# Kernel tuning notes

Measured on AMD Instinct MI355X. Metric: run time of the kernel, lower is better.

## Reference

```python
import jax, jax.numpy as jnp
import numpy as np

EPS = 1e-5

def rmsnorm(x, w, eps=EPS):
    # torch-style RMSNorm: x / rms(x) * weight
    return x * jax.lax.rsqrt(jnp.mean(x * x, axis=-1, keepdims=True) + eps) * w

def setup_inputs() -> dict:
    key = jax.random.key(0)
    k1, k2 = jax.random.split(key)
    B, T, D, Q, K = 8, 1024, 1024, 8, 4096
    d = D // Q
    x = jax.random.normal(k1, (B, T, D), dtype=jnp.float32)
    codebooks = jax.random.normal(k2, (Q, K, d), dtype=jnp.float32)
    input_norm_w = jnp.ones((D,), dtype=jnp.float32)
    output_norm_w = jnp.ones((D,), dtype=jnp.float32)
    return {"x": x, "codebooks": codebooks,
            "input_norm_w": input_norm_w, "output_norm_w": output_norm_w}

def reference(x, codebooks, input_norm_w, output_norm_w):
    B, T, D = x.shape
    Q, K, d = codebooks.shape
    xn = rmsnorm(x, input_norm_w)
    xq = xn.reshape(B, T, Q, d)  # split hidden into Q sub-vectors
    # squared euclidean distances (argmin equal to cdist argmin)
    x2 = jnp.sum(xq * xq, axis=-1, keepdims=True)          # [B,T,Q,1]
    c2 = jnp.sum(codebooks * codebooks, axis=-1)           # [Q,K]
    xc = jnp.einsum('btqd,qkd->btqk', xq, codebooks)       # [B,T,Q,K]
    d2 = x2 - 2.0 * xc + c2[None, None]                    # [B,T,Q,K]
    idx = jnp.argmin(d2, axis=-1)                          # [B,T,Q] int
    # gather nearest code per quantizer: equivalent of stacked embedding lookups
    quant = codebooks[jnp.arange(Q)[None, None, :], idx]   # [B,T,Q,d]
    quant = quant.reshape(B, T, D)
    out = rmsnorm(quant, output_norm_w)
    return out, idx
```

## Files before the change

### kernel.cpp

```cpp
#include <hip/hip_runtime.h>
#include <math.h>
#include <float.h>

#define Q_     8
#define K_     4096
#define dd_    128
#define D_     1024
#define ROWS   8192
#define NCHUNK 64
#define NCH_L  32
#define TAU    0.02f

typedef __attribute__((ext_vector_type(8))) _Float16 f16x8;
typedef __attribute__((ext_vector_type(4))) float f32x4;
typedef __attribute__((ext_vector_type(4))) unsigned int u32x4;

typedef const __attribute__((address_space(1))) unsigned int* gas_p;
typedef __attribute__((address_space(3))) unsigned int* las_p;

__device__ inline unsigned f2u(float x) { union { float f; unsigned u; } v; v.f = x; return v.u; }
__device__ inline float u2f(unsigned x) { union { unsigned u; float f; } v; v.u = x; return v.f; }
__device__ inline unsigned short f2h(float x) {
    union { _Float16 h; unsigned short u; } v; v.h = (_Float16)x; return v.u;
}
__device__ inline unsigned umin_(unsigned a, unsigned b) { return a < b ? a : b; }
__device__ inline unsigned umax_(unsigned a, unsigned b) { return a > b ? a : b; }
__device__ inline unsigned fflip(float x) {
    unsigned u = f2u(x);
    return (u & 0x80000000u) ? ~u : (u | 0x80000000u);
}
__device__ inline unsigned long long shfl_xor_u64(unsigned long long v, int m) {
    unsigned lo = (unsigned)v, hi = (unsigned)(v >> 32);
    lo = __shfl_xor(lo, m, 64);
    hi = __shfl_xor(hi, m, 64);
    return ((unsigned long long)hi << 32) | lo;
}

__global__ void k_prep(const float* __restrict__ cb, const float* __restrict__ x,
                       const float* __restrict__ w, float* __restrict__ xn,
                       unsigned short* __restrict__ panels, float* __restrict__ c2h,
                       float* __restrict__ x2h, int* __restrict__ cntF, int* __restrict__ cntS) {
    const int bid = blockIdx.x, t = threadIdx.x;
    if (bid == 0 && t == 0) { *cntF = 0; *cntS = 0; }
    if (bid < NCHUNK * Q_) {
        int c = bid & 63, q = bid >> 6;
        const float* src = cb + ((size_t)q * K_ + c * 64) * dd_;
        unsigned short* dst = panels + (size_t)(q * NCHUNK + c) * 8192;
        #pragma unroll
        for (int i = 0; i < 4; i++) {
            int sid = i * 256 + t;
            int n = sid >> 4, j = sid & 15;
            const float* sp = src + n * dd_ + j * 8;
            f32x4 v0 = *(const f32x4*)sp;
            f32x4 v1 = *(const f32x4*)(sp + 4);
            float xs[8] = {v0.x, v0.y, v0.z, v0.w, v1.x, v1.y, v1.z, v1.w};
            unsigned short hb[8];
            float ss = 0.0f;
            #pragma unroll
            for (int e = 0; e < 8; e++) {
                float xv = -xs[e];
                ss = fmaf(xv, xv, ss);
                hb[e] = f2h(xv);
            }
            int slot = j ^ (n & 15);
            u32x4 H;
            H.x = (unsigned)hb[0] | ((unsigned)hb[1] << 16);
            H.y = (unsigned)hb[2] | ((unsigned)hb[3] << 16);
            H.z = (unsigned)hb[4] | ((unsigned)hb[5] << 16);
            H.w = (unsigned)hb[6] | ((unsigned)hb[7] << 16);
            *(u32x4*)&dst[(n * 16 + slot) * 8] = H;
            ss += __shfl_xor(ss, 1, 64);
            ss += __shfl_xor(ss, 2, 64);
            ss += __shfl_xor(ss, 4, 64);
            ss += __shfl_xor(ss, 8, 64);
            if (j == 0) c2h[q * K_ + c * 64 + n] = 0.5f * ss;
        }
    } else {
        int row = bid - NCHUNK * Q_;
        const float4 v = *(const float4*)(x + (size_t)row * D_ + t * 4);
        float ss = v.x * v.x + v.y * v.y + v.z * v.z + v.w * v.w;
        #pragma unroll
        for (int o = 32; o > 0; o >>= 1) ss += __shfl_xor(ss, o, 64);
        __shared__ float acc[4];
        if ((t & 63) == 0) acc[t >> 6] = ss;
        __syncthreads();
        float tot = (acc[0] + acc[1]) + (acc[2] + acc[3]);
        float sc  = 1.0f / sqrtf(tot * (1.0f / D_) + 1e-5f);
        const float4 wv = *(const float4*)(w + t * 4);
        float4 o;
        o.x = v.x * sc * wv.x; o.y = v.y * sc * wv.y;
        o.z = v.z * sc * wv.z; o.w = v.w * sc * wv.w;
        *(float4*)(xn + (size_t)row * D_ + t * 4) = o;
        float so = o.x * o.x + o.y * o.y + o.z * o.z + o.w * o.w;
        so += __shfl_xor(so, 1, 64);
        so += __shfl_xor(so, 2, 64);
        so += __shfl_xor(so, 4, 64);
        so += __shfl_xor(so, 8, 64);
        so += __shfl_xor(so, 16, 64);
        if ((t & 31) == 0) x2h[row * Q_ + (t >> 5)] = 0.5f * so;
    }
}

__launch_bounds__(256, 2)
__global__ void k_dist(const float* __restrict__ xn, const unsigned short* __restrict__ panels,
                       const float* __restrict__ c2h, const float* __restrict__ x2h,
                       unsigned* __restrict__ recs) {
    __shared__ char smem[36864];

    const int t    = threadIdx.x;
    const int lane = t & 63, wave = t >> 6;
    const int wm = wave >> 1, wn = wave & 1;
    const int col = lane & 15, quad = lane >> 4;
    const int q = blockIdx.y;
    const int z = blockIdx.z;
    const int row0 = blockIdx.x * 128;

    f16x8 ah[4][4], al[4][4];
    #pragma unroll
    for (int mt = 0; mt < 4; mt++) {
        #pragma unroll
        for (int kt = 0; kt < 4; kt++) {
            const float* ap = xn + (size_t)(row0 + wm * 64 + mt * 16 + col) * D_
                              + q * dd_ + kt * 32 + quad * 8;
            f32x4 v0 = *(const f32x4*)ap;
            f32x4 v1 = *(const f32x4*)(ap + 4);
            #pragma unroll
            for (int e = 0; e < 8; e++) {
                float xv = (e < 4) ? v0[e] : v1[e - 4];
                _Float16 h = (_Float16)xv;
                float r = xv - (float)h;
                ah[mt][kt][e] = h;
                al[mt][kt][e] = (_Float16)r;
            }
        }
    }

    f32x4 x2v[4];
    #pragma unroll
    for (int mt = 0; mt < 4; mt++)
        #pragma unroll
        for (int r = 0; r < 4; r++)
            x2v[mt][r] = x2h[(size_t)(row0 + wm * 64 + mt * 16 + quad * 4 + r) * Q_ + q];

    unsigned m1[16], m2[16];
    #pragma unroll
    for (int i = 0; i < 16; i++) { m1[i] = 0xFFFFFFFFu; m2[i] = 0xFFFFFFFFu; }

    const size_t panq = (size_t)q * NCHUNK * 8192 + (size_t)z * NCH_L * 8192;
    const float* c2hq = c2h + q * K_ + z * (NCH_L * 64);

    {
        const unsigned short* src = panels + panq;
        #pragma unroll
        for (int i = 0; i < 4; i++) {
            int boff = i * 4096 + t * 16;
            __builtin_amdgcn_global_load_lds((gas_p)((const char*)src + boff),
                                             (las_p)(smem + boff), 16, 0, 0);
        }
    }
    float ch0 = c2hq[wn * 32 + col];
    float ch1 = c2hq[wn * 32 + col + 16];

    for (int c = 0; c < NCH_L; c++) {
        __syncthreads();
        if (c + 1 < NCH_L) {
            const unsigned short* src = panels + panq + (size_t)(c + 1) * 8192;
            char* stage = smem + ((c + 1) & 1) * 16384;
            #pragma unroll
            for (int i = 0; i < 4; i++) {
                int boff = i * 4096 + t * 16;
                __builtin_amdgcn_global_load_lds((gas_p)((const char*)src + boff),
                                                 (las_p)(stage + boff), 16, 0, 0);
            }
        }
        float ch0n = 0.0f, ch1n = 0.0f;
        if (c + 1 < NCH_L) {
            ch0n = c2hq[(c + 1) * 64 + wn * 32 + col];
            ch1n = c2hq[(c + 1) * 64 + wn * 32 + col + 16];
        }
        const char* cbuf = smem + (c & 1) * 16384;

        f32x4 acc[4][2];
        #pragma unroll
        for (int mt = 0; mt < 4; mt++) {
            acc[mt][0] = x2v[mt] + ch0;
            acc[mt][1] = x2v[mt] + ch1;
        }

        #pragma unroll
        for (int kt = 0; kt < 4; kt++) {
            const int sw = ((quad + kt * 4) ^ col) * 16;
            const int a0 = (wn * 32 + col) * 256 + sw;
            const int a1 = a0 + 4096;
            f16x8 b0 = *(const f16x8*)(cbuf + a0);
            f16x8 b1 = *(const f16x8*)(cbuf + a1);
            #pragma unroll
            for (int mt = 0; mt < 4; mt++) {
                acc[mt][0] = __builtin_amdgcn_mfma_f32_16x16x32_f16(ah[mt][kt], b0, acc[mt][0], 0, 0, 0);
                acc[mt][0] = __builtin_amdgcn_mfma_f32_16x16x32_f16(al[mt][kt], b0, acc[mt][0], 0, 0, 0);
                acc[mt][1] = __builtin_amdgcn_mfma_f32_16x16x32_f16(ah[mt][kt], b1, acc[mt][1], 0, 0, 0);
                acc[mt][1] = __builtin_amdgcn_mfma_f32_16x16x32_f16(al[mt][kt], b1, acc[mt][1], 0, 0, 0);
            }
        }

        const unsigned tg0 = (unsigned)((z * NCH_L + c) << 1), tg1 = tg0 | 1u;
        #pragma unroll
        for (int mt = 0; mt < 4; mt++) {
            #pragma unroll
            for (int r = 0; r < 4; r++) {
                const int sl = mt * 4 + r;
                unsigned p0 = (f2u(acc[mt][0][r]) & 0xFFFFFF80u) | tg0;
                unsigned p1 = (f2u(acc[mt][1][r]) & 0xFFFFFF80u) | tg1;
                unsigned pmin = umin_(p0, p1), pmax = umax_(p0, p1);
                m2[sl] = umin_(umin_(m2[sl], umax_(m1[sl], pmin)), pmax);
                m1[sl] = umin_(m1[sl], pmin);
            }
        }
        ch0 = ch0n; ch1 = ch1n;
    }

    __syncthreads();
    unsigned* rm1 = (unsigned*)smem;
    unsigned* rm2 = (unsigned*)(smem + 16896);
    #pragma unroll
    for (int mt = 0; mt < 4; mt++) {
        #pragma unroll
        for (int r = 0; r < 4; r++) {
            int sl = mt * 4 + r;
            int row_l = wm * 64 + mt * 16 + quad * 4 + r;
            int e = wn * 16 + col;
            rm1[row_l * 33 + e] = m1[sl];
            rm2[row_l * 33 + e] = m2[sl];
        }
    }
    __syncthreads();
    if (t < 128) {
        unsigned b1 = 0xFFFFFFFFu;
        int be = 0;
        for (int e = 0; e < 32; e++) {
            unsigned v1 = rm1[t * 33 + e];
            if (v1 < b1) { b1 = v1; be = e; }
        }
        float f1  = u2f(b1 & 0xFFFFFF80u);
        float thr = f1 + TAU;
        int ns = 0, fb = 0;
        unsigned sv0 = 0xFFFFFFFFu, sk0 = 0, sv1 = 0xFFFFFFFFu, sk1 = 0;
        for (int e = 0; e < 32; e++) {
            unsigned v2m = rm2[t * 33 + e] & 0xFFFFFF80u;
            if (u2f(v2m) < thr) fb = 1;
            if (e != be) {
                unsigned v1 = rm1[t * 33 + e];
                unsigned vm = v1 & 0xFFFFFF80u;
                if (u2f(vm) < thr) {
                    unsigned tg = v1 & 0x7Fu;
                    unsigned kk = ((tg >> 1) << 6) | (((unsigned)e >> 4) << 5)
                                | ((tg & 1u) << 4) | ((unsigned)e & 15u);
                    if (ns == 0)      { sv0 = vm; sk0 = kk; }
                    else if (ns == 1) { sv1 = vm; sk1 = kk; }
                    ns++;
                }
            }
        }
        if (ns > 2) fb = 1;
        unsigned tg1x = b1 & 0x7Fu;
        unsigned k1 = ((tg1x >> 1) << 6) | (((unsigned)be >> 4) << 5)
                    | ((tg1x & 1u) << 4) | ((unsigned)be & 15u);
        int item = (row0 + t) * Q_ + q;
        unsigned* rec = recs + ((size_t)item * 2 + z) * 8;
        rec[0] = b1 & 0xFFFFFF80u;
        rec[1] = k1;
        rec[2] = (unsigned)ns | ((unsigned)fb << 8);
        rec[3] = 0;
        rec[4] = sv0; rec[5] = sk0;
        rec[6] = sv1; rec[7] = sk1;
    }
}

__global__ void k_merge(const unsigned* __restrict__ recs, int* __restrict__ idxi,
                        float* __restrict__ idxf, int* __restrict__ listF, int* __restrict__ cntF,
                        int* __restrict__ srl, int* __restrict__ cntS,
                        unsigned long long* __restrict__ resc) {
    int item = blockIdx.x * blockDim.x + threadIdx.x;
    if (item >= ROWS * Q_) return;
    const unsigned* ra = recs + (size_t)item * 16;
    const unsigned* rb = ra + 8;
    unsigned m1a = ra[0], m1b = rb[0];
    bool awin = m1a <= m1b;
    unsigned mw = awin ? m1a : m1b;
    unsigned kw = awin ? ra[1] : rb[1];
    unsigned ml = awin ? m1b : m1a;
    unsigned kl = awin ? rb[1] : ra[1];
    float thr = u2f(mw) + TAU;
    int fb = (int)(((ra[2] | rb[2]) >> 8) & 1u);

    bool q0 = u2f(ml) < thr;
    int nsa = (int)(ra[2] & 0xFFu), nsb = (int)(rb[2] & 0xFFu);
    bool qa0 = (nsa > 0) && (u2f(ra[4]) < thr);
    bool qa1 = (nsa > 1) && (u2f(ra[6]) < thr);
    bool qb0 = (nsb > 0) && (u2f(rb[4]) < thr);
    bool qb1 = (nsb > 1) && (u2f(rb[6]) < thr);
    int nr = (int)q0 + (int)qa0 + (int)qa1 + (int)qb0 + (int)qb1;

    idxi[item] = (int)kw;
    idxf[item] = (float)kw;
    if (fb) {
        resc[item] = 0xFFFFFFFFFFFFFFFFull;
        int p = atomicAdd(cntF, 1);
        listF[p] = item;
    } else if (nr > 0) {
        int p = atomicAdd(cntS, 1);
        int* e = srl + (size_t)p * 8;
        e[0] = item; e[1] = nr + 1; e[2] = (int)kw;
        int o = 3;
        if (q0)  e[o++] = (int)kl;
        if (qa0) e[o++] = (int)ra[5];
        if (qa1) e[o++] = (int)ra[7];
        if (qb0) e[o++] = (int)rb[5];
        if (qb1) e[o++] = (int)rb[7];
    }
}

__global__ void k_rescue(const float* __restrict__ xn, const float* __restrict__ cb,
                         const float* __restrict__ c2h, const int* __restrict__ listF,
                         const int* __restrict__ cntF, const int* __restrict__ srl,
                         const int* __restrict__ cntS,
                         unsigned long long* __restrict__ resc,
                         int* __restrict__ idxi, float* __restrict__ idxf) {
    __shared__ float xq[dd_];
    __shared__ unsigned long long kshare[8];
    const int t = threadIdx.x;
    if (blockIdx.x < 2048) {
        const int n = *cntF;
        const int seg = blockIdx.x & 7;
        for (int ii = blockIdx.x >> 3; ii < n; ii += 256) {
            __syncthreads();
            int item = listF[ii];
            int rg = item >> 3, q = item & 7;
            if (t < dd_) xq[t] = xn[(size_t)rg * D_ + q * dd_ + t];
            __syncthreads();
            unsigned long long best = 0xFFFFFFFFFFFFFFFFull;
            #pragma unroll
            for (int i = 0; i < 2; i++) {
                int k = seg * 512 + i * 256 + t;
                const float* cp = cb + ((size_t)q * K_ + k) * dd_;
                float dot = 0.0f;
                #pragma unroll 8
                for (int d = 0; d < dd_; d += 4) {
                    f32x4 cv = *(const f32x4*)(cp + d);
                    dot = fmaf(cv.x, xq[d],     dot);
                    dot = fmaf(cv.y, xq[d + 1], dot);
                    dot = fmaf(cv.z, xq[d + 2], dot);
                    dot = fmaf(cv.w, xq[d + 3], dot);
                }
                float s = c2h[q * K_ + k] - dot;
                unsigned long long key = ((unsigned long long)fflip(s) << 32) | (unsigned)k;
                best = best < key ? best : key;
            }
            #pragma unroll
            for (int o = 32; o > 0; o >>= 1) {
                unsigned long long other = shfl_xor_u64(best, o);
                best = best < other ? best : other;
            }
            if ((t & 63) == 0) kshare[t >> 6] = best;
            __syncthreads();
            if (t == 0) {
                unsigned long long b = kshare[0];
                b = b < kshare[1] ? b : kshare[1];
                b = b < kshare[2] ? b : kshare[2];
                b = b < kshare[3] ? b : kshare[3];
                atomicMin(&resc[item], b);
            }
        }
    } else {
        const int n = *cntS;
        for (int ii = (int)blockIdx.x - 2048; ii < n; ii += 2048) {
            __syncthreads();
            const int* e = srl + (size_t)ii * 8;
            int item = e[0], nc = e[1];
            int rg = item >> 3, q = item & 7;
            if (t < dd_) xq[t] = xn[(size_t)rg * D_ + q * dd_ + t];
            __syncthreads();
            int g = t >> 5, l = t & 31;
            unsigned long long key = 0xFFFFFFFFFFFFFFFFull;
            if (g < nc) {
                int k = e[2 + g];
                const float* cp = cb + ((size_t)q * K_ + k) * dd_ + l * 4;
                f32x4 cv = *(const f32x4*)cp;
                float dot = cv.x * xq[l * 4]     + cv.y * xq[l * 4 + 1]
                          + cv.z * xq[l * 4 + 2] + cv.w * xq[l * 4 + 3];
                dot += __shfl_xor(dot, 16, 64);
                dot += __shfl_xor(dot, 8, 64);
                dot += __shfl_xor(dot, 4, 64);
                dot += __shfl_xor(dot, 2, 64);
                dot += __shfl_xor(dot, 1, 64);
                float s = c2h[q * K_ + k] - dot;
                key = ((unsigned long long)fflip(s) << 32) | (unsigned)k;
            }
            if (l == 0) kshare[g] = key;
            __syncthreads();
            if (t == 0) {
                unsigned long long b = kshare[0];
                #pragma unroll
                for (int gg = 1; gg < 8; gg++) b = b < kshare[gg] ? b : kshare[gg];
                int k = (int)(unsigned)(b & 0xFFFFFFFFull);
                idxi[item] = k;
                idxf[item] = (float)k;
            }
        }
    }
}

__global__ void k_fin(const int* __restrict__ listF, const int* __restrict__ cntF,
                      const unsigned long long* __restrict__ resc,
                      int* __restrict__ idxi, float* __restrict__ idxf) {
    const int n = *cntF;
    for (int i = blockIdx.x * blockDim.x + threadIdx.x; i < n; i += gridDim.x * blockDim.x) {
        int item = listF[i];
        int k = (int)(unsigned)(resc[item] & 0xFFFFFFFFull);
        idxi[item] = k;
        idxf[item] = (float)k;
    }
}

__global__ void k_out(const float* __restrict__ cb, const int* __restrict__ idx_i,
                      const float* __restrict__ w, float* __restrict__ out) {
    int row = blockIdx.x;
    int t   = threadIdx.x;
    __shared__ int   sidx[Q_];
    __shared__ float acc[4];
    if (t < Q_) sidx[t] = idx_i[row * Q_ + t];
    __syncthreads();
    int col = t * 4;
    int q   = col >> 7;
    int dc  = col & 127;
    const float4 v = *(const float4*)(cb + ((size_t)q * K_ + sidx[q]) * dd_ + dc);
    float ss = v.x * v.x + v.y * v.y + v.z * v.z + v.w * v.w;
    #pragma unroll
    for (int o = 32; o > 0; o >>= 1) ss += __shfl_xor(ss, o, 64);
    if ((t & 63) == 0) acc[t >> 6] = ss;
    __syncthreads();
    float tot = (acc[0] + acc[1]) + (acc[2] + acc[3]);
    float sc  = 1.0f / sqrtf(tot * (1.0f / D_) + 1e-5f);
    const float4 wv = *(const float4*)(w + col);
    float4 o;
    o.x = v.x * sc * wv.x; o.y = v.y * sc * wv.y;
    o.z = v.z * sc * wv.z; o.w = v.w * sc * wv.w;
    *(float4*)(out + (size_t)row * D_ + col) = o;
}

extern "C" void kernel_launch(void* const* d_in, const int* in_sizes, int n_in,
                              void* d_out, int out_size, void* d_ws, size_t ws_size,
                              hipStream_t stream) {
    const float* x     = (const float*)d_in[0];
    const float* cb    = (const float*)d_in[1];
    const float* w_in  = (const float*)d_in[2];
    const float* w_out = (const float*)d_in[3];

    float* out  = (float*)d_out;
    float* idxf = out + (size_t)ROWS * D_;

    unsigned short* panels = (unsigned short*)d_ws;
    float* c2h  = (float*)((char*)d_ws + (8u << 20));
    float* x2h  = c2h + Q_ * K_;
    unsigned long long* resc = (unsigned long long*)(x2h + (size_t)ROWS * Q_);
    int*   idxi = (int*)(resc + (size_t)ROWS * Q_);
    int*   listF = idxi + ROWS * Q_;
    unsigned* recs = (unsigned*)(listF + ROWS * Q_);
    int*   srl  = (int*)(recs + (size_t)ROWS * Q_ * 16);
    int*   cntF = srl + (size_t)ROWS * Q_ * 8;
    int*   cntS = cntF + 1;

    k_prep  <<<dim3(NCHUNK * Q_ + ROWS), 256, 0, stream>>>(cb, x, w_in, out, panels, c2h, x2h, cntF, cntS);
    k_dist  <<<dim3(ROWS / 128, Q_, 2),  256, 0, stream>>>(out, panels, c2h, x2h, recs);
    k_merge <<<dim3(ROWS * Q_ / 256),    256, 0, stream>>>(recs, idxi, idxf, listF, cntF, srl, cntS, resc);
    k_rescue<<<dim3(4096),               256, 0, stream>>>(out, cb, c2h, listF, cntF, srl, cntS, resc, idxi, idxf);
    k_fin   <<<dim3(64),                 256, 0, stream>>>(listF, cntF, resc, idxi, idxf);
    k_out   <<<dim3(ROWS),               256, 0, stream>>>(cb, idxi, w_out, out);
}
```

Before: 246.7 us.

## Triple-buffer codebook panels with explicit vmcnt waits and stage c2 in LDS

Changes the k_dist main loop from double-buffered to triple-buffered LDS staging, prefetching two chunks ahead. It replaces __syncthreads with manual s_waitcnt vmcnt and s_barrier so one chunk's loads stay in flight across the barrier. The c2 norms are copied into LDS once and added after the MFMA chain rather than in the accumulator init, and MFMA sections get raised wave priority. Shared memory grows from 36KB to 56KB, which may reduce occupancy below the two-blocks launch bound.

```diff
diff --git a/kernel.cpp b/kernel.cpp
--- a/kernel.cpp
+++ b/kernel.cpp
@@ -105,7 +105,7 @@
 __global__ void k_dist(const float* __restrict__ xn, const unsigned short* __restrict__ panels,
                        const float* __restrict__ c2h, const float* __restrict__ x2h,
                        unsigned* __restrict__ recs) {
-    __shared__ char smem[36864];
+    __shared__ char smem[57344];
 
     const int t    = threadIdx.x;
     const int lane = t & 63, wave = t >> 6;
@@ -147,48 +147,61 @@
     for (int i = 0; i < 16; i++) { m1[i] = 0xFFFFFFFFu; m2[i] = 0xFFFFFFFFu; }
 
     const size_t panq = (size_t)q * NCHUNK * 8192 + (size_t)z * NCH_L * 8192;
-    const float* c2hq = c2h + q * K_ + z * (NCH_L * 64);
+    const float* c2s = (const float*)(smem + 49152);
 
     {
-        const unsigned short* src = panels + panq;
-        #pragma unroll
-        for (int i = 0; i < 4; i++) {
+        const char* c2src = (const char*)(c2h + (size_t)q * K_ + (size_t)z * (NCH_L * 64));
+        #pragma unroll
+        for (int i = 0; i < 2; i++) {
             int boff = i * 4096 + t * 16;
-            __builtin_amdgcn_global_load_lds((gas_p)((const char*)src + boff),
-                                             (las_p)(smem + boff), 16, 0, 0);
-        }
-    }
-    float ch0 = c2hq[wn * 32 + col];
-    float ch1 = c2hq[wn * 32 + col + 16];
-
-    for (int c = 0; c < NCH_L; c++) {
-        __syncthreads();
-        if (c + 1 < NCH_L) {
-            const unsigned short* src = panels + panq + (size_t)(c + 1) * 8192;
-            char* stage = smem + ((c + 1) & 1) * 16384;
+            __builtin_amdgcn_global_load_lds((gas_p)(c2src + boff),
+                                             (las_p)(smem + 49152 + boff), 16, 0, 0);
+        }
+        #pragma unroll
+        for (int b = 0; b < 2; b++) {
+            const char* src = (const char*)(panels + panq + (size_t)b * 8192);
             #pragma unroll
             for (int i = 0; i < 4; i++) {
                 int boff = i * 4096 + t * 16;
-                __builtin_amdgcn_global_load_lds((gas_p)((const char*)src + boff),
+                __builtin_amdgcn_global_load_lds((gas_p)(src + boff),
+                                                 (las_p)(smem + b * 16384 + boff), 16, 0, 0);
+            }
+        }
+    }
+    asm volatile("s_waitcnt vmcnt(4)" ::: "memory");
+    __builtin_amdgcn_s_barrier();
+
+    for (int c = 0; c < NCH_L; c++) {
+        const char* cbuf = smem + (c % 3) * 16384;
+        if (c + 2 < NCH_L) {
+            const char* src = (const char*)(panels + panq + (size_t)(c + 2) * 8192);
+            char* stage = smem + ((c + 2) % 3) * 16384;
+            #pragma unroll
+            for (int i = 0; i < 4; i++) {
+                int boff = i * 4096 + t * 16;
+                __builtin_amdgcn_global_load_lds((gas_p)(src + boff),
                                                  (las_p)(stage + boff), 16, 0, 0);
             }
         }
-        float ch0n = 0.0f, ch1n = 0.0f;
-        if (c + 1 < NCH_L) {
-            ch0n = c2hq[(c + 1) * 64 + wn * 32 + col];
-            ch1n = c2hq[(c + 1) * 64 + wn * 32 + col + 16];
-        }
-        const char* cbuf = smem + (c & 1) * 16384;
 
         f32x4 acc[4][2];
-        #pragma unroll
-        for (int mt = 0; mt < 4; mt++) {
-            acc[mt][0] = x2v[mt] + ch0;
-            acc[mt][1] = x2v[mt] + ch1;
-        }
-
-        #pragma unroll
-        for (int kt = 0; kt < 4; kt++) {
+        __builtin_amdgcn_s_setprio(1);
+        {
+            const int sw = (quad ^ col) * 16;
+            const int a0 = (wn * 32 + col) * 256 + sw;
+            const int a1 = a0 + 4096;
+            f16x8 b0 = *(const f16x8*)(cbuf + a0);
+            f16x8 b1 = *(const f16x8*)(cbuf + a1);
+            #pragma unroll
+            for (int mt = 0; mt < 4; mt++) {
+                acc[mt][0] = __builtin_amdgcn_mfma_f32_16x16x32_f16(ah[mt][0], b0, x2v[mt], 0, 0, 0);
+                acc[mt][0] = __builtin_amdgcn_mfma_f32_16x16x32_f16(al[mt][0], b0, acc[mt][0], 0, 0, 0);
+                acc[mt][1] = __builtin_amdgcn_mfma_f32_16x16x32_f16(ah[mt][0], b1, x2v[mt], 0, 0, 0);
+                acc[mt][1] = __builtin_amdgcn_mfma_f32_16x16x32_f16(al[mt][0], b1, acc[mt][1], 0, 0, 0);
+            }
+        }
+        #pragma unroll
+        for (int kt = 1; kt < 4; kt++) {
             const int sw = ((quad + kt * 4) ^ col) * 16;
             const int a0 = (wn * 32 + col) * 256 + sw;
             const int a1 = a0 + 4096;
@@ -202,21 +215,30 @@
                 acc[mt][1] = __builtin_amdgcn_mfma_f32_16x16x32_f16(al[mt][kt], b1, acc[mt][1], 0, 0, 0);
             }
         }
-
+        __builtin_amdgcn_s_setprio(0);
+
+        const float ch0 = c2s[c * 64 + wn * 32 + col];
+        const float ch1 = c2s[c * 64 + wn * 32 + col + 16];
         const unsigned tg0 = (unsigned)((z * NCH_L + c) << 1), tg1 = tg0 | 1u;
         #pragma unroll
         for (int mt = 0; mt < 4; mt++) {
             #pragma unroll
             for (int r = 0; r < 4; r++) {
                 const int sl = mt * 4 + r;
-                unsigned p0 = (f2u(acc[mt][0][r]) & 0xFFFFFF80u) | tg0;
-                unsigned p1 = (f2u(acc[mt][1][r]) & 0xFFFFFF80u) | tg1;
+                unsigned p0 = (f2u(acc[mt][0][r] + ch0) & 0xFFFFFF80u) | tg0;
+                unsigned p1 = (f2u(acc[mt][1][r] + ch1) & 0xFFFFFF80u) | tg1;
                 unsigned pmin = umin_(p0, p1), pmax = umax_(p0, p1);
                 m2[sl] = umin_(umin_(m2[sl], umax_(m1[sl], pmin)), pmax);
                 m1[sl] = umin_(m1[sl], pmin);
             }
         }
-        ch0 = ch0n; ch1 = ch1n;
+
+        if (c + 2 < NCH_L) {
+            asm volatile("s_waitcnt vmcnt(4) lgkmcnt(0)" ::: "memory");
+        } else {
+            asm volatile("s_waitcnt vmcnt(0) lgkmcnt(0)" ::: "memory");
+        }
+        __builtin_amdgcn_s_barrier();
     }
 
     __syncthreads();
```

Result: slower. 261.3 us (+5.9%).

## Drop codebook split and merge kernel; software-pipeline MFMA with argmin packing

Applied to the files above, without the earlier changes.

The distance kernel no longer splits the codebook across two z-blocks. Each block now scans all 64 chunks and writes the final index and rescue lists directly, so the k_merge kernel and its record buffer go away. The c2 norms are staged into shared memory, and the argmin packing of the previous chunk is interleaved with the MFMAs of the current chunk using two alternating accumulator sets. The grid is halved to 512 blocks, which may reduce parallelism on a large GPU. Shared memory grows to 48KB and register pressure rises from the double accumulators.

```diff
diff --git a/kernel.cpp b/kernel.cpp
--- a/kernel.cpp
+++ b/kernel.cpp
@@ -8,7 +8,6 @@
 #define D_     1024
 #define ROWS   8192
 #define NCHUNK 64
-#define NCH_L  32
 #define TAU    0.02f
 
 typedef __attribute__((ext_vector_type(8))) _Float16 f16x8;
@@ -34,6 +33,10 @@
     lo = __shfl_xor(lo, m, 64);
     hi = __shfl_xor(hi, m, 64);
     return ((unsigned long long)hi << 32) | lo;
+}
+__device__ inline unsigned dec_k(unsigned v, int e) {
+    unsigned tg = v & 0x7Fu;
+    return ((tg >> 1) << 6) | (((unsigned)e >> 4) << 5) | ((tg & 1u) << 4) | ((unsigned)e & 15u);
 }
 
 __global__ void k_prep(const float* __restrict__ cb, const float* __restrict__ x,
@@ -101,18 +104,70 @@
     }
 }
 
+#define STAGE(CN) do {                                                                   \
+    const char* src_ = (const char*)(panels + panq + (size_t)(CN) * 8192);               \
+    char* stg_ = smem + ((CN) & 1) * 16384;                                              \
+    _Pragma("unroll")                                                                    \
+    for (int i_ = 0; i_ < 4; i_++) {                                                     \
+        int boff_ = i_ * 4096 + t * 16;                                                  \
+        __builtin_amdgcn_global_load_lds((gas_p)(src_ + boff_), (las_p)(stg_ + boff_),   \
+                                         16, 0, 0);                                      \
+    }                                                                                    \
+} while (0)
+
+#define PACK_Q(ACC, MT, TG0, TG1, CH0, CH1) do {                                         \
+    _Pragma("unroll")                                                                    \
+    for (int r_ = 0; r_ < 4; r_++) {                                                     \
+        const int sl_ = (MT) * 4 + r_;                                                   \
+        unsigned p0_ = (f2u(ACC[MT][0][r_] + (CH0)) & 0xFFFFFF80u) | (TG0);              \
+        unsigned p1_ = (f2u(ACC[MT][1][r_] + (CH1)) & 0xFFFFFF80u) | (TG1);              \
+        unsigned pmin_ = umin_(p0_, p1_), pmax_ = umax_(p0_, p1_);                       \
+        m2[sl_] = umin_(umin_(m2[sl_], umax_(m1[sl_], pmin_)), pmax_);                   \
+        m1[sl_] = umin_(m1[sl_], pmin_);                                                 \
+    }                                                                                    \
+} while (0)
+
+#define PHASE(C, ACCW, ACCP) do {                                                        \
+    __syncthreads();                                                                     \
+    if ((C) + 1 < NCHUNK) STAGE((C) + 1);                                                \
+    const char* cbuf_ = smem + ((C) & 1) * 16384;                                        \
+    const int cp_ = (C) - 1;                                                             \
+    const float pch0_ = c2s[cp_ * 64 + wn * 32 + col];                                   \
+    const float pch1_ = c2s[cp_ * 64 + wn * 32 + col + 16];                              \
+    const unsigned ptg0_ = ((unsigned)cp_ << 1) & 0x7Fu, ptg1_ = ptg0_ | 1u;             \
+    _Pragma("unroll")                                                                    \
+    for (int kt_ = 0; kt_ < 4; kt_++) {                                                  \
+        const int sw_ = ((quad + kt_ * 4) ^ col) * 16;                                   \
+        const int a0_ = (wn * 32 + col) * 256 + sw_;                                     \
+        f16x8 b0_ = *(const f16x8*)(cbuf_ + a0_);                                        \
+        f16x8 b1_ = *(const f16x8*)(cbuf_ + a0_ + 4096);                                 \
+        _Pragma("unroll")                                                                \
+        for (int mt_ = 0; mt_ < 4; mt_++) {                                              \
+            f32x4 cin0_ = (kt_ == 0) ? x2v[mt_] : ACCW[mt_][0];                          \
+            f32x4 cin1_ = (kt_ == 0) ? x2v[mt_] : ACCW[mt_][1];                          \
+            ACCW[mt_][0] = __builtin_amdgcn_mfma_f32_16x16x32_f16(ah[mt_][kt_], b0_, cin0_, 0, 0, 0); \
+            ACCW[mt_][0] = __builtin_amdgcn_mfma_f32_16x16x32_f16(al[mt_][kt_], b0_, ACCW[mt_][0], 0, 0, 0); \
+            ACCW[mt_][1] = __builtin_amdgcn_mfma_f32_16x16x32_f16(ah[mt_][kt_], b1_, cin1_, 0, 0, 0); \
+            ACCW[mt_][1] = __builtin_amdgcn_mfma_f32_16x16x32_f16(al[mt_][kt_], b1_, ACCW[mt_][1], 0, 0, 0); \
+        }                                                                                \
+        PACK_Q(ACCP, kt_, ptg0_, ptg1_, pch0_, pch1_);                                   \
+    }                                                                                    \
+} while (0)
+
 __launch_bounds__(256, 2)
 __global__ void k_dist(const float* __restrict__ xn, const unsigned short* __restrict__ panels,
                        const float* __restrict__ c2h, const float* __restrict__ x2h,
-                       unsigned* __restrict__ recs) {
-    __shared__ char smem[36864];
+                       int* __restrict__ idxi, float* __restrict__ idxf,
+                       int* __restrict__ listF, int* __restrict__ cntF,
+                       int* __restrict__ srl, int* __restrict__ cntS,
+                       unsigned long long* __restrict__ resc) {
+    __shared__ char smem[49152];
 
     const int t    = threadIdx.x;
     const int lane = t & 63, wave = t >> 6;
     const int wm = wave >> 1, wn = wave & 1;
     const int col = lane & 15, quad = lane >> 4;
     const int q = blockIdx.y;
-    const int z = blockIdx.z;
     const int row0 = blockIdx.x * 128;
 
     f16x8 ah[4][4], al[4][4];
@@ -146,77 +201,37 @@
     #pragma unroll
     for (int i = 0; i < 16; i++) { m1[i] = 0xFFFFFFFFu; m2[i] = 0xFFFFFFFFu; }
 
-    const size_t panq = (size_t)q * NCHUNK * 8192 + (size_t)z * NCH_L * 8192;
-    const float* c2hq = c2h + q * K_ + z * (NCH_L * 64);
+    const size_t panq = (size_t)q * NCHUNK * 8192;
+    const float* c2s = (const float*)(smem + 32768);
 
     {
-        const unsigned short* src = panels + panq;
+        const char* c2src = (const char*)(c2h + (size_t)q * K_);
         #pragma unroll
         for (int i = 0; i < 4; i++) {
             int boff = i * 4096 + t * 16;
-            __builtin_amdgcn_global_load_lds((gas_p)((const char*)src + boff),
-                                             (las_p)(smem + boff), 16, 0, 0);
-        }
-    }
-    float ch0 = c2hq[wn * 32 + col];
-    float ch1 = c2hq[wn * 32 + col + 16];
-
-    for (int c = 0; c < NCH_L; c++) {
-        __syncthreads();
-        if (c + 1 < NCH_L) {
-            const unsigned short* src = panels + panq + (size_t)(c + 1) * 8192;
-            char* stage = smem + ((c + 1) & 1) * 16384;
-            #pragma unroll
-            for (int i = 0; i < 4; i++) {
-                int boff = i * 4096 + t * 16;
-                __builtin_amdgcn_global_load_lds((gas_p)((const char*)src + boff),
-                                                 (las_p)(stage + boff), 16, 0, 0);
-            }
-        }
-        float ch0n = 0.0f, ch1n = 0.0f;
-        if (c + 1 < NCH_L) {
-            ch0n = c2hq[(c + 1) * 64 + wn * 32 + col];
-            ch1n = c2hq[(c + 1) * 64 + wn * 32 + col + 16];
-        }
-        const char* cbuf = smem + (c & 1) * 16384;
-
-        f32x4 acc[4][2];
-        #pragma unroll
-        for (int mt = 0; mt < 4; mt++) {
-            acc[mt][0] = x2v[mt] + ch0;
-            acc[mt][1] = x2v[mt] + ch1;
-        }
-
-        #pragma unroll
-        for (int kt = 0; kt < 4; kt++) {
-            const int sw = ((quad + kt * 4) ^ col) * 16;
-            const int a0 = (wn * 32 + col) * 256 + sw;
-            const int a1 = a0 + 4096;
-            f16x8 b0 = *(const f16x8*)(cbuf + a0);
-            f16x8 b1 = *(const f16x8*)(cbuf + a1);
-            #pragma unroll
-            for (int mt = 0; mt < 4; mt++) {
-                acc[mt][0] = __builtin_amdgcn_mfma_f32_16x16x32_f16(ah[mt][kt], b0, acc[mt][0], 0, 0, 0);
-                acc[mt][0] = __builtin_amdgcn_mfma_f32_16x16x32_f16(al[mt][kt], b0, acc[mt][0], 0, 0, 0);
-                acc[mt][1] = __builtin_amdgcn_mfma_f32_16x16x32_f16(ah[mt][kt], b1, acc[mt][1], 0, 0, 0);
-                acc[mt][1] = __builtin_amdgcn_mfma_f32_16x16x32_f16(al[mt][kt], b1, acc[mt][1], 0, 0, 0);
-            }
-        }
-
-        const unsigned tg0 = (unsigned)((z * NCH_L + c) << 1), tg1 = tg0 | 1u;
-        #pragma unroll
-        for (int mt = 0; mt < 4; mt++) {
-            #pragma unroll
-            for (int r = 0; r < 4; r++) {
-                const int sl = mt * 4 + r;
-                unsigned p0 = (f2u(acc[mt][0][r]) & 0xFFFFFF80u) | tg0;
-                unsigned p1 = (f2u(acc[mt][1][r]) & 0xFFFFFF80u) | tg1;
-                unsigned pmin = umin_(p0, p1), pmax = umax_(p0, p1);
-                m2[sl] = umin_(umin_(m2[sl], umax_(m1[sl], pmin)), pmax);
-                m1[sl] = umin_(m1[sl], pmin);
-            }
-        }
-        ch0 = ch0n; ch1 = ch1n;
+            __builtin_amdgcn_global_load_lds((gas_p)(c2src + boff),
+                                             (las_p)(smem + 32768 + boff), 16, 0, 0);
+        }
+        STAGE(0);
+    }
+
+    f32x4 accA[4][2], accB[4][2];
+    const f32x4 big = {1e30f, 1e30f, 1e30f, 1e30f};
+    #pragma unroll
+    for (int mt = 0; mt < 4; mt++) { accB[mt][0] = big; accB[mt][1] = big; }
+
+    for (int cc = 0; cc < NCHUNK; cc += 2) {
+        PHASE(cc,     accA, accB);
+        PHASE(cc + 1, accB, accA);
+    }
+    {
+        const float pch0_ = c2s[63 * 64 + wn * 32 + col];
+        const float pch1_ = c2s[63 * 64 + wn * 32 + col + 16];
+        const unsigned ptg0_ = (unsigned)(63 << 1), ptg1_ = ptg0_ | 1u;
+        PACK_Q(accB, 0, ptg0_, ptg1_, pch0_, pch1_);
+        PACK_Q(accB, 1, ptg0_, ptg1_, pch0_, pch1_);
+        PACK_Q(accB, 2, ptg0_, ptg1_, pch0_, pch1_);
+        PACK_Q(accB, 3, ptg0_, ptg1_, pch0_, pch1_);
     }
 
     __syncthreads();
@@ -241,82 +256,35 @@
             unsigned v1 = rm1[t * 33 + e];
             if (v1 < b1) { b1 = v1; be = e; }
         }
-        float f1  = u2f(b1 & 0xFFFFFF80u);
-        float thr = f1 + TAU;
+        float thr = u2f(b1 & 0xFFFFFF80u) + TAU;
         int ns = 0, fb = 0;
-        unsigned sv0 = 0xFFFFFFFFu, sk0 = 0, sv1 = 0xFFFFFFFFu, sk1 = 0;
+        unsigned long long candpack = 0;
         for (int e = 0; e < 32; e++) {
-            unsigned v2m = rm2[t * 33 + e] & 0xFFFFFF80u;
-            if (u2f(v2m) < thr) fb = 1;
+            if (u2f(rm2[t * 33 + e] & 0xFFFFFF80u) < thr) fb = 1;
             if (e != be) {
                 unsigned v1 = rm1[t * 33 + e];
-                unsigned vm = v1 & 0xFFFFFF80u;
-                if (u2f(vm) < thr) {
-                    unsigned tg = v1 & 0x7Fu;
-                    unsigned kk = ((tg >> 1) << 6) | (((unsigned)e >> 4) << 5)
-                                | ((tg & 1u) << 4) | ((unsigned)e & 15u);
-                    if (ns == 0)      { sv0 = vm; sk0 = kk; }
-                    else if (ns == 1) { sv1 = vm; sk1 = kk; }
+                if (u2f(v1 & 0xFFFFFF80u) < thr) {
+                    if (ns < 5) candpack |= (unsigned long long)dec_k(v1, e) << (12 * ns);
                     ns++;
                 }
             }
         }
-        if (ns > 2) fb = 1;
-        unsigned tg1x = b1 & 0x7Fu;
-        unsigned k1 = ((tg1x >> 1) << 6) | (((unsigned)be >> 4) << 5)
-                    | ((tg1x & 1u) << 4) | ((unsigned)be & 15u);
+        if (ns > 5) fb = 1;
+        unsigned k1 = dec_k(b1, be);
         int item = (row0 + t) * Q_ + q;
-        unsigned* rec = recs + ((size_t)item * 2 + z) * 8;
-        rec[0] = b1 & 0xFFFFFF80u;
-        rec[1] = k1;
-        rec[2] = (unsigned)ns | ((unsigned)fb << 8);
-        rec[3] = 0;
-        rec[4] = sv0; rec[5] = sk0;
-        rec[6] = sv1; rec[7] = sk1;
-    }
-}
-
-__global__ void k_merge(const unsigned* __restrict__ recs, int* __restrict__ idxi,
-                        float* __restrict__ idxf, int* __restrict__ listF, int* __restrict__ cntF,
-                        int* __restrict__ srl, int* __restrict__ cntS,
-                        unsigned long long* __restrict__ resc) {
-    int item = blockIdx.x * blockDim.x + threadIdx.x;
-    if (item >= ROWS * Q_) return;
-    const unsigned* ra = recs + (size_t)item * 16;
-    const unsigned* rb = ra + 8;
-    unsigned m1a = ra[0], m1b = rb[0];
-    bool awin = m1a <= m1b;
-    unsigned mw = awin ? m1a : m1b;
-    unsigned kw = awin ? ra[1] : rb[1];
-    unsigned ml = awin ? m1b : m1a;
-    unsigned kl = awin ? rb[1] : ra[1];
-    float thr = u2f(mw) + TAU;
-    int fb = (int)(((ra[2] | rb[2]) >> 8) & 1u);
-
-    bool q0 = u2f(ml) < thr;
-    int nsa = (int)(ra[2] & 0xFFu), nsb = (int)(rb[2] & 0xFFu);
-    bool qa0 = (nsa > 0) && (u2f(ra[4]) < thr);
-    bool qa1 = (nsa > 1) && (u2f(ra[6]) < thr);
-    bool qb0 = (nsb > 0) && (u2f(rb[4]) < thr);
-    bool qb1 = (nsb > 1) && (u2f(rb[6]) < thr);
-    int nr = (int)q0 + (int)qa0 + (int)qa1 + (int)qb0 + (int)qb1;
-
-    idxi[item] = (int)kw;
-    idxf[item] = (float)kw;
-    if (fb) {
-        resc[item] = 0xFFFFFFFFFFFFFFFFull;
-        int p = atomicAdd(cntF, 1);
-        listF[p] = item;
-    } else if (nr > 0) {
-        int p = atomicAdd(cntS, 1);
-        int* e = srl + (size_t)p * 8;
-        e[0] = item; e[1] = nr + 1; e[2] = (int)kw;
-        int o = 3;
-        if (q0)  e[o++] = (int)kl;
-        if (qa0) e[o++] = (int)ra[5];
-        if (qa1) e[o++] = (int)ra[7];
-        if (qb0) e[o++] = (int)rb[5];
-        if (qb1) e[o++] = (int)rb[7];
+        idxi[item] = (int)k1;
+        idxf[item] = (float)k1;
+        if (fb) {
+            resc[item] = 0xFFFFFFFFFFFFFFFFull;
+            int p = atomicAdd(cntF, 1);
+            listF[p] = item;
+        } else if (ns > 0) {
+            int p = atomicAdd(cntS, 1);
+            int* e8 = srl + (size_t)p * 8;
+            e8[0] = item; e8[1] = ns + 1; e8[2] = (int)k1;
+            for (int i = 0; i < ns; i++)
+                e8[3 + i] = (int)((candpack >> (12 * i)) & 0xFFFu);
+        }
     }
 }
 
@@ -465,14 +433,12 @@
     unsigned long long* resc = (unsigned long long*)(x2h + (size_t)ROWS * Q_);
     int*   idxi = (int*)(resc + (size_t)ROWS * Q_);
     int*   listF = idxi + ROWS * Q_;
-    unsigned* recs = (unsigned*)(listF + ROWS * Q_);
-    int*   srl  = (int*)(recs + (size_t)ROWS * Q_ * 16);
+    int*   srl  = listF + ROWS * Q_;
     int*   cntF = srl + (size_t)ROWS * Q_ * 8;
     int*   cntS = cntF + 1;
 
     k_prep  <<<dim3(NCHUNK * Q_ + ROWS), 256, 0, stream>>>(cb, x, w_in, out, panels, c2h, x2h, cntF, cntS);
-    k_dist  <<<dim3(ROWS / 128, Q_, 2),  256, 0, stream>>>(out, panels, c2h, x2h, recs);
-    k_merge <<<dim3(ROWS * Q_ / 256),    256, 0, stream>>>(recs, idxi, idxf, listF, cntF, srl, cntS, resc);
+    k_dist  <<<dim3(ROWS / 128, Q_),     256, 0, stream>>>(out, panels, c2h, x2h, idxi, idxf, listF, cntF, srl, cntS, resc);
     k_rescue<<<dim3(4096),               256, 0, stream>>>(out, cb, c2h, listF, cntF, srl, cntS, resc, idxi, idxf);
     k_fin   <<<dim3(64),                 256, 0, stream>>>(listF, cntF, resc, idxi, idxf);
     k_out   <<<dim3(ROWS),               256, 0, stream>>>(cb, idxi, w_out, out);
```

Result: slower. 273.6 us (+10.9%).
